# Kernel tuning notes

Measured on AMD Instinct MI355X. Metric: run time of the kernel, lower is better.

## Reference

```python
import jax, jax.numpy as jnp
import numpy as np
import math

B, N, C, H = 8, 128, 256, 8  # batch, nodes (n==m required by module), dim, heads
HD = C // H


def setup_inputs() -> dict:
    key = jax.random.key(0)
    ks = jax.random.split(key, 20)
    p = lambda k, shape: jax.random.normal(k, shape, dtype=jnp.float32) * 0.02
    inp = {
        "mol_annot": jax.random.normal(ks[0], (B, N, C), dtype=jnp.float32),
        "prot_annot": jax.random.normal(ks[1], (B, N, C), dtype=jnp.float32),
        "mol_adj": jax.random.normal(ks[2], (B, N, N, C), dtype=jnp.float32),
        "prot_adj": jax.random.normal(ks[3], (B, N, N, C), dtype=jnp.float32),
        # linear layer params (y = x @ W + b)
        "Wq": p(ks[4], (C, C)), "bq": jnp.zeros((C,), jnp.float32),
        "Wk": p(ks[5], (C, C)), "bk": jnp.zeros((C,), jnp.float32),
        "Wv": p(ks[6], (C, C)), "bv": jnp.zeros((C,), jnp.float32),
        "Wka": p(ks[7], (C, C)), "bka": jnp.zeros((C,), jnp.float32),
        "Wva": p(ks[8], (C, C)), "bva": jnp.zeros((C,), jnp.float32),
        "Wond": p(ks[9], (C, C)), "bond": jnp.zeros((C,), jnp.float32),
        "Woed": p(ks[10], (C, C)), "boed": jnp.zeros((C,), jnp.float32),
    }
    return inp


def reference(mol_annot, prot_annot, mol_adj, prot_adj,
              Wq, bq, Wk, bk, Wv, bv, Wka, bka, Wva, bva,
              Wond, bond, Woed, boed):
    b, n, c = mol_annot.shape
    h, hd = H, C // H
    inv_sqrt_dim = 1.0 / math.sqrt(c)

    q = (mol_annot @ Wq + bq).reshape(b, n, h, hd)        # [b,m,h,hd]
    k = (prot_annot @ Wk + bk).reshape(b, n, h, hd)       # [b,n,h,hd]
    v = (mol_annot @ Wv + bv).reshape(b, n, h, hd)        # [b,n,h,hd]
    mol_e = (mol_adj @ Wva + bva).reshape(b, n, n, h, hd)   # [b,m,n,h,hd]
    prot_e = (prot_adj @ Wka + bka).reshape(b, n, n, h, hd)  # [b,m,n,h,hd]

    # elementwise q*k score (full head_dim retained), gated by edge features
    attn = (q[:, :, None] * k[:, None]) * inv_sqrt_dim     # [b,m,n,h,hd]
    attn = attn * (prot_e + 1.0) * mol_e

    # edge output projection from pre-softmax scores
    mol_adj_out = attn.reshape(b, n, n, c) @ Woed + boed   # [b,m,n,c]

    # softmax over key axis (dim=2), then weighted value sum
    a = jax.nn.softmax(attn, axis=2)                       # [b,m,n,h,hd]
    node = (a * v[:, None]).sum(axis=2).reshape(b, n, c)   # [b,m,c]
    mol_annot_out = node @ Wond + bond

    return (mol_annot_out, prot_annot, mol_adj_out, prot_adj)
```

## Files before the change

kernel.cpp:

```cpp
#include <hip/hip_runtime.h>
#include <stdint.h>

constexpr int kB = 8;
constexpr int kN = 128;
constexpr int kC = 256;
#define ATTN_SCALE 0.0625f

using half8 = __attribute__((ext_vector_type(8))) _Float16;
using half4 = __attribute__((ext_vector_type(4))) _Float16;
using f32x4 = __attribute__((ext_vector_type(4))) float;

__global__ __launch_bounds__(256) void qkv_kernel(
    const float* __restrict__ mol_annot,
    const float* __restrict__ prot_annot,
    const float* __restrict__ Wq, const float* __restrict__ bq,
    const float* __restrict__ Wk, const float* __restrict__ bk,
    const float* __restrict__ Wv, const float* __restrict__ bv,
    float* __restrict__ qf, _Float16* __restrict__ kf16, float* __restrict__ vf)
{
    const int row = blockIdx.x;
    const int t   = threadIdx.x;

    __shared__ float sm[kC];
    __shared__ float sp[kC];
    sm[t] = mol_annot[row * kC + t];
    sp[t] = prot_annot[row * kC + t];
    __syncthreads();

    float aq = bq[t];
    float ak = bk[t];
    float av = bv[t];
    for (int c = 0; c < kC; ++c) {
        const float m = sm[c];
        const float p = sp[c];
        aq += m * Wq[c * kC + t];
        ak += p * Wk[c * kC + t];
        av += m * Wv[c * kC + t];
    }
    qf[row * kC + t]   = aq;
    kf16[row * kC + t] = (_Float16)ak;
    vf[row * kC + t]   = av;
}

__global__ __launch_bounds__(256) void pack_w_kernel(
    const float* __restrict__ Wva, const float* __restrict__ Wka,
    const float* __restrict__ Woed,
    _Float16* __restrict__ p_wva, _Float16* __restrict__ p_wka,
    _Float16* __restrict__ p_woed)
{
    const int blk = blockIdx.x;
    const int mat = blk >> 8;
    const int k   = blk & 255;
    const int n   = threadIdx.x;

    const float* src = (mat == 0) ? Wva : (mat == 1) ? Wka : Woed;
    _Float16*    dst = (mat == 0) ? p_wva : (mat == 1) ? p_wka : p_woed;

    const float w   = src[k * kC + n];
    const int nblk  = n >> 4;
    const int kblk  = k >> 5;
    const int lane  = (((k >> 3) & 3) << 4) | (n & 15);
    const int i     = k & 7;
    dst[(size_t)(((nblk * 8) + kblk) * 64 + lane) * 8 + i] = (_Float16)w;
}

__global__ __launch_bounds__(512, 2) void main_kernel(
    const float* __restrict__ mol_adj,
    const float* __restrict__ prot_adj,
    const float* __restrict__ bka, const float* __restrict__ bva,
    const float* __restrict__ Wond, const float* __restrict__ bond,
    const float* __restrict__ boed,
    const _Float16* __restrict__ p_wva, const _Float16* __restrict__ p_wka,
    const _Float16* __restrict__ p_woed,
    const float* __restrict__ qf, const _Float16* __restrict__ kf16,
    const float* __restrict__ vf,
    float* __restrict__ out_node,
    float* __restrict__ out_edge)
{
    const int bm   = blockIdx.x;
    const int b    = bm >> 7;
    const int tid  = threadIdx.x;
    const int lane = tid & 63;
    const int wave = tid >> 6;
    const int wm   = wave >> 2;
    const int wn   = wave & 3;
    const int lr   = lane & 15;
    const int lk   = (lane >> 4) << 3;
    const int lg4  = (lane >> 4) << 2;

    __shared__ __align__(16) _Float16 s_stage[2][kN][136];
    _Float16 (*s_attn)[264] = reinterpret_cast<_Float16 (*)[264]>(&s_stage[0][0][0]);
    __shared__ float s_red[6][kC];
    __shared__ float s_node[kC];

    float qs[4], bva_c[4], bka_c[4], boed_c[4];
    int   colv[4];
    #pragma unroll
    for (int ni = 0; ni < 4; ++ni) {
        const int c = wn * 64 + ni * 16 + lr;
        colv[ni]   = c;
        qs[ni]     = qf[(size_t)bm * kC + c] * ATTN_SCALE;
        bva_c[ni]  = bva[c];
        bka_c[ni]  = bka[c];
        boed_c[ni] = boed[c];
    }

    const float* madj = mol_adj  + (size_t)bm * kN * kC;
    const float* padj = prot_adj + (size_t)bm * kN * kC;

    f32x4 accme[4][4], accpe[4][4];
    #pragma unroll
    for (int mi = 0; mi < 4; ++mi)
        #pragma unroll
        for (int ni = 0; ni < 4; ++ni) { accme[mi][ni] = (f32x4)0.0f; accpe[mi][ni] = (f32x4)0.0f; }

    for (int kc = 0; kc < 2; ++kc) {
        #pragma unroll
        for (int v = 0; v < 8; ++v) {
            const int e   = tid + v * 512;
            const int row = e >> 5;
            const int c4  = e & 31;
            const float4 fm = *(const float4*)(madj + row * kC + kc * 128 + c4 * 4);
            const float4 fp = *(const float4*)(padj + row * kC + kc * 128 + c4 * 4);
            half4 hm, hp;
            hm[0] = (_Float16)fm.x; hm[1] = (_Float16)fm.y;
            hm[2] = (_Float16)fm.z; hm[3] = (_Float16)fm.w;
            hp[0] = (_Float16)fp.x; hp[1] = (_Float16)fp.y;
            hp[2] = (_Float16)fp.z; hp[3] = (_Float16)fp.w;
            *(half4*)&s_stage[0][row][c4 * 4] = hm;
            *(half4*)&s_stage[1][row][c4 * 4] = hp;
        }
        __syncthreads();

        #pragma unroll
        for (int kk = 0; kk < 4; ++kk) {
            const int kblk = kc * 4 + kk;
            half8 am[4], ap[4], bvf[4], bkf[4];
            #pragma unroll
            for (int mi = 0; mi < 4; ++mi) {
                const int r = wm * 64 + mi * 16 + lr;
                am[mi] = *(const half8*)&s_stage[0][r][kk * 32 + lk];
                ap[mi] = *(const half8*)&s_stage[1][r][kk * 32 + lk];
            }
            #pragma unroll
            for (int ni = 0; ni < 4; ++ni) {
                const size_t off = ((size_t)((wn * 4 + ni) * 8 + kblk) * 64 + lane) * 8;
                bvf[ni] = *(const half8*)&p_wva[off];
                bkf[ni] = *(const half8*)&p_wka[off];
            }
            #pragma unroll
            for (int mi = 0; mi < 4; ++mi)
                #pragma unroll
                for (int ni = 0; ni < 4; ++ni) {
                    accme[mi][ni] = __builtin_amdgcn_mfma_f32_16x16x32_f16(am[mi], bvf[ni], accme[mi][ni], 0, 0, 0);
                    accpe[mi][ni] = __builtin_amdgcn_mfma_f32_16x16x32_f16(ap[mi], bkf[ni], accpe[mi][ni], 0, 0, 0);
                }
        }
        __syncthreads();
    }

    const _Float16* kbase = kf16 + (size_t)b * kN * kC;
    #pragma unroll
    for (int mi = 0; mi < 4; ++mi) {
        #pragma unroll
        for (int ni = 0; ni < 4; ++ni) {
            #pragma unroll
            for (int r = 0; r < 4; ++r) {
                const int row = wm * 64 + mi * 16 + lg4 + r;
                const float kvv = (float)kbase[row * kC + colv[ni]];
                const float me  = accme[mi][ni][r] + bva_c[ni];
                const float pe  = accpe[mi][ni][r] + bka_c[ni];
                const float a   = qs[ni] * kvv * (pe + 1.0f) * me;
                s_attn[row][colv[ni]] = (_Float16)a;
            }
        }
    }
    __syncthreads();

    f32x4 acco[4][4];
    #pragma unroll
    for (int mi = 0; mi < 4; ++mi)
        #pragma unroll
        for (int ni = 0; ni < 4; ++ni) acco[mi][ni] = (f32x4)0.0f;

    #pragma unroll
    for (int kk = 0; kk < 8; ++kk) {
        half8 aa[4], bo[4];
        #pragma unroll
        for (int mi = 0; mi < 4; ++mi)
            aa[mi] = *(const half8*)&s_attn[wm * 64 + mi * 16 + lr][kk * 32 + lk];
        #pragma unroll
        for (int ni = 0; ni < 4; ++ni)
            bo[ni] = *(const half8*)&p_woed[((size_t)((wn * 4 + ni) * 8 + kk) * 64 + lane) * 8];
        #pragma unroll
        for (int mi = 0; mi < 4; ++mi)
            #pragma unroll
            for (int ni = 0; ni < 4; ++ni)
                acco[mi][ni] = __builtin_amdgcn_mfma_f32_16x16x32_f16(aa[mi], bo[ni], acco[mi][ni], 0, 0, 0);
    }

    float* oe = out_edge + (size_t)bm * kN * kC;
    #pragma unroll
    for (int mi = 0; mi < 4; ++mi)
        #pragma unroll
        for (int ni = 0; ni < 4; ++ni)
            #pragma unroll
            for (int r = 0; r < 4; ++r) {
                const int row = wm * 64 + mi * 16 + lg4 + r;
                oe[(size_t)row * kC + colv[ni]] = acco[mi][ni][r] + boed_c[ni];
            }

    {
        const int c  = tid & 255;
        const int hh = tid >> 8;
        const int r0 = hh * 64;

        float mx = -1.0e30f;
        #pragma unroll 4
        for (int r = 0; r < 64; ++r) mx = fmaxf(mx, (float)s_attn[r0 + r][c]);
        s_red[hh][c] = mx;
        __syncthreads();
        mx = fmaxf(s_red[0][c], s_red[1][c]);

        const float* vbase = vf + (size_t)b * kN * kC;
        float ssum = 0.0f, sacc = 0.0f;
        #pragma unroll 4
        for (int r = 0; r < 64; ++r) {
            const float a = (float)s_attn[r0 + r][c];
            const float e = __expf(a - mx);
            ssum += e;
            sacc += e * vbase[(size_t)(r0 + r) * kC + c];
        }
        s_red[2 + hh][c] = ssum;
        s_red[4 + hh][c] = sacc;
        __syncthreads();
        if (tid < 256) {
            s_node[tid] = (s_red[4][tid] + s_red[5][tid]) /
                          (s_red[2][tid] + s_red[3][tid]);
        }
        __syncthreads();
    }

    if (tid < 256) {
        float acc = bond[tid];
        const float4* sn4 = reinterpret_cast<const float4*>(s_node);
        for (int c4 = 0; c4 < 64; ++c4) {
            const float4 nv = sn4[c4];
            acc += nv.x * Wond[(c4 * 4 + 0) * kC + tid];
            acc += nv.y * Wond[(c4 * 4 + 1) * kC + tid];
            acc += nv.z * Wond[(c4 * 4 + 2) * kC + tid];
            acc += nv.w * Wond[(c4 * 4 + 3) * kC + tid];
        }
        out_node[(size_t)bm * kC + tid] = acc;
    }
}

extern "C" void kernel_launch(void* const* d_in, const int* in_sizes, int n_in,
                              void* d_out, int out_size, void* d_ws, size_t ws_size,
                              hipStream_t stream)
{
    const float* mol_annot  = (const float*)d_in[0];
    const float* prot_annot = (const float*)d_in[1];
    const float* mol_adj    = (const float*)d_in[2];
    const float* prot_adj   = (const float*)d_in[3];
    const float* Wq  = (const float*)d_in[4];
    const float* bq  = (const float*)d_in[5];
    const float* Wk  = (const float*)d_in[6];
    const float* bk  = (const float*)d_in[7];
    const float* Wv  = (const float*)d_in[8];
    const float* bv  = (const float*)d_in[9];
    const float* Wka = (const float*)d_in[10];
    const float* bka = (const float*)d_in[11];
    const float* Wva = (const float*)d_in[12];
    const float* bva = (const float*)d_in[13];
    const float* Wond = (const float*)d_in[14];
    const float* bond = (const float*)d_in[15];
    const float* Woed = (const float*)d_in[16];
    const float* boed = (const float*)d_in[17];

    float*    qf    = (float*)d_ws;
    float*    vf    = qf + (size_t)kB * kN * kC;
    _Float16* kf16  = (_Float16*)(vf + (size_t)kB * kN * kC);
    _Float16* p_wva = kf16 + (size_t)kB * kN * kC;
    _Float16* p_wka = p_wva + (size_t)kC * kC;
    _Float16* p_woed = p_wka + (size_t)kC * kC;

    float* out  = (float*)d_out;
    float* out0 = out;
    float* out1 = out + (size_t)kB * kN * kC;
    float* out2 = out + (size_t)2 * kB * kN * kC;
    float* out3 = out2 + (size_t)kB * kN * kN * kC;

    hipMemcpyAsync(out1, prot_annot, (size_t)kB * kN * kC * sizeof(float),
                   hipMemcpyDeviceToDevice, stream);
    hipMemcpyAsync(out3, prot_adj, (size_t)kB * kN * kN * kC * sizeof(float),
                   hipMemcpyDeviceToDevice, stream);

    qkv_kernel<<<dim3(kB * kN), dim3(256), 0, stream>>>(
        mol_annot, prot_annot, Wq, bq, Wk, bk, Wv, bv, qf, kf16, vf);

    pack_w_kernel<<<dim3(3 * kC), dim3(256), 0, stream>>>(
        Wva, Wka, Woed, p_wva, p_wka, p_woed);

    main_kernel<<<dim3(kB * kN), dim3(512), 0, stream>>>(
        mol_adj, prot_adj, bka, bva, Wond, bond, boed,
        p_wva, p_wka, p_woed, qf, kf16, vf, out0, out2);
}
```

Baseline: 678.7 us.

## Fuse passthrough copies into kernels and serialize edge GEMMs to raise occupancy

Drops the two device-to-device memcpys and writes the prot_annot and prot_adj passthrough outputs from inside qkv_kernel and main_kernel while those tensors are already being read. This saves a separate full read of the large prot_adj tensor. The main kernel now runs the prot_e and mol_e projections one after the other with a single accumulator set and a small 32-wide staging buffer. This cuts registers and LDS so launch bounds can go from 2 to 4 blocks. Edge output is staged through LDS for coalesced float4 stores, and the k-loop now has more barriers per block.

```diff
diff --git a/kernel.cpp b/kernel.cpp
--- a/kernel.cpp
+++ b/kernel.cpp
@@ -16,15 +16,18 @@
     const float* __restrict__ Wq, const float* __restrict__ bq,
     const float* __restrict__ Wk, const float* __restrict__ bk,
     const float* __restrict__ Wv, const float* __restrict__ bv,
-    float* __restrict__ qf, _Float16* __restrict__ kf16, float* __restrict__ vf)
+    float* __restrict__ qf, _Float16* __restrict__ kf16, float* __restrict__ vf,
+    float* __restrict__ out1)
 {
     const int row = blockIdx.x;
     const int t   = threadIdx.x;
 
     __shared__ float sm[kC];
     __shared__ float sp[kC];
+    const float pv = prot_annot[row * kC + t];
     sm[t] = mol_annot[row * kC + t];
-    sp[t] = prot_annot[row * kC + t];
+    sp[t] = pv;
+    out1[row * kC + t] = pv;
     __syncthreads();
 
     float aq = bq[t];
@@ -64,7 +67,7 @@
     dst[(size_t)(((nblk * 8) + kblk) * 64 + lane) * 8 + i] = (_Float16)w;
 }
 
-__global__ __launch_bounds__(512, 2) void main_kernel(
+__global__ __launch_bounds__(512, 4) void main_kernel(
     const float* __restrict__ mol_adj,
     const float* __restrict__ prot_adj,
     const float* __restrict__ bka, const float* __restrict__ bva,
@@ -75,7 +78,8 @@
     const float* __restrict__ qf, const _Float16* __restrict__ kf16,
     const float* __restrict__ vf,
     float* __restrict__ out_node,
-    float* __restrict__ out_edge)
+    float* __restrict__ out_edge,
+    float* __restrict__ out3)
 {
     const int bm   = blockIdx.x;
     const int b    = bm >> 7;
@@ -88,127 +92,135 @@
     const int lk   = (lane >> 4) << 3;
     const int lg4  = (lane >> 4) << 2;
 
-    __shared__ __align__(16) _Float16 s_stage[2][kN][136];
-    _Float16 (*s_attn)[264] = reinterpret_cast<_Float16 (*)[264]>(&s_stage[0][0][0]);
-    __shared__ float s_red[6][kC];
-    __shared__ float s_node[kC];
-
-    float qs[4], bva_c[4], bka_c[4], boed_c[4];
-    int   colv[4];
-    #pragma unroll
-    for (int ni = 0; ni < 4; ++ni) {
-        const int c = wn * 64 + ni * 16 + lr;
-        colv[ni]   = c;
-        qs[ni]     = qf[(size_t)bm * kC + c] * ATTN_SCALE;
-        bva_c[ni]  = bva[c];
-        bka_c[ni]  = bka[c];
-        boed_c[ni] = boed[c];
-    }
+    __shared__ __align__(16) _Float16 s_attn[kN][264];
+    __shared__ __align__(16) _Float16 s_stage[kN][40];
+    float (*s_red)[kC] = reinterpret_cast<float (*)[kC]>(&s_stage[0][0]);
+    float (*s_oe)[260] = reinterpret_cast<float (*)[260]>(&s_attn[0][0]);
 
     const float* madj = mol_adj  + (size_t)bm * kN * kC;
     const float* padj = prot_adj + (size_t)bm * kN * kC;
-
-    f32x4 accme[4][4], accpe[4][4];
+    float*       o3   = out3     + (size_t)bm * kN * kC;
+
+    const int srow = tid >> 3;
+    const int sc4  = (tid & 7) * 4;
+
+    f32x4 acc[4][4];
+
     #pragma unroll
     for (int mi = 0; mi < 4; ++mi)
         #pragma unroll
-        for (int ni = 0; ni < 4; ++ni) { accme[mi][ni] = (f32x4)0.0f; accpe[mi][ni] = (f32x4)0.0f; }
-
-    for (int kc = 0; kc < 2; ++kc) {
-        #pragma unroll
-        for (int v = 0; v < 8; ++v) {
-            const int e   = tid + v * 512;
-            const int row = e >> 5;
-            const int c4  = e & 31;
-            const float4 fm = *(const float4*)(madj + row * kC + kc * 128 + c4 * 4);
-            const float4 fp = *(const float4*)(padj + row * kC + kc * 128 + c4 * 4);
-            half4 hm, hp;
-            hm[0] = (_Float16)fm.x; hm[1] = (_Float16)fm.y;
-            hm[2] = (_Float16)fm.z; hm[3] = (_Float16)fm.w;
-            hp[0] = (_Float16)fp.x; hp[1] = (_Float16)fp.y;
-            hp[2] = (_Float16)fp.z; hp[3] = (_Float16)fp.w;
-            *(half4*)&s_stage[0][row][c4 * 4] = hm;
-            *(half4*)&s_stage[1][row][c4 * 4] = hp;
-        }
-        __syncthreads();
-
-        #pragma unroll
-        for (int kk = 0; kk < 4; ++kk) {
-            const int kblk = kc * 4 + kk;
-            half8 am[4], ap[4], bvf[4], bkf[4];
-            #pragma unroll
-            for (int mi = 0; mi < 4; ++mi) {
-                const int r = wm * 64 + mi * 16 + lr;
-                am[mi] = *(const half8*)&s_stage[0][r][kk * 32 + lk];
-                ap[mi] = *(const half8*)&s_stage[1][r][kk * 32 + lk];
-            }
-            #pragma unroll
-            for (int ni = 0; ni < 4; ++ni) {
-                const size_t off = ((size_t)((wn * 4 + ni) * 8 + kblk) * 64 + lane) * 8;
-                bvf[ni] = *(const half8*)&p_wva[off];
-                bkf[ni] = *(const half8*)&p_wka[off];
-            }
+        for (int ni = 0; ni < 4; ++ni) acc[mi][ni] = (f32x4)0.0f;
+
+    for (int kc = 0; kc < 8; ++kc) {
+        #pragma unroll
+        for (int v = 0; v < 2; ++v) {
+            const int r = srow + v * 64;
+            const float4 f = *(const float4*)(padj + r * kC + kc * 32 + sc4);
+            *(float4*)(o3 + r * kC + kc * 32 + sc4) = f;
+            half4 h;
+            h[0] = (_Float16)f.x; h[1] = (_Float16)f.y;
+            h[2] = (_Float16)f.z; h[3] = (_Float16)f.w;
+            *(half4*)&s_stage[r][sc4] = h;
+        }
+        __syncthreads();
+
+        half8 af[4];
+        #pragma unroll
+        for (int mi = 0; mi < 4; ++mi)
+            af[mi] = *(const half8*)&s_stage[wm * 64 + mi * 16 + lr][lk];
+        #pragma unroll
+        for (int ni = 0; ni < 4; ++ni) {
+            const half8 bf = *(const half8*)&p_wka[((size_t)((wn * 4 + ni) * 8 + kc) * 64 + lane) * 8];
+            #pragma unroll
+            for (int mi = 0; mi < 4; ++mi)
+                acc[mi][ni] = __builtin_amdgcn_mfma_f32_16x16x32_f16(af[mi], bf, acc[mi][ni], 0, 0, 0);
+        }
+        __syncthreads();
+    }
+
+    #pragma unroll
+    for (int ni = 0; ni < 4; ++ni) {
+        const int col = wn * 64 + ni * 16 + lr;
+        const float bk_c = bka[col] + 1.0f;
+        #pragma unroll
+        for (int mi = 0; mi < 4; ++mi)
+            #pragma unroll
+            for (int r = 0; r < 4; ++r)
+                s_attn[wm * 64 + mi * 16 + lg4 + r][col] = (_Float16)(acc[mi][ni][r] + bk_c);
+    }
+
+    #pragma unroll
+    for (int mi = 0; mi < 4; ++mi)
+        #pragma unroll
+        for (int ni = 0; ni < 4; ++ni) acc[mi][ni] = (f32x4)0.0f;
+
+    for (int kc = 0; kc < 8; ++kc) {
+        #pragma unroll
+        for (int v = 0; v < 2; ++v) {
+            const int r = srow + v * 64;
+            const float4 f = *(const float4*)(madj + r * kC + kc * 32 + sc4);
+            half4 h;
+            h[0] = (_Float16)f.x; h[1] = (_Float16)f.y;
+            h[2] = (_Float16)f.z; h[3] = (_Float16)f.w;
+            *(half4*)&s_stage[r][sc4] = h;
+        }
+        __syncthreads();
+
+        half8 af[4];
+        #pragma unroll
+        for (int mi = 0; mi < 4; ++mi)
+            af[mi] = *(const half8*)&s_stage[wm * 64 + mi * 16 + lr][lk];
+        #pragma unroll
+        for (int ni = 0; ni < 4; ++ni) {
+            const half8 bf = *(const half8*)&p_wva[((size_t)((wn * 4 + ni) * 8 + kc) * 64 + lane) * 8];
+            #pragma unroll
+            for (int mi = 0; mi < 4; ++mi)
+                acc[mi][ni] = __builtin_amdgcn_mfma_f32_16x16x32_f16(af[mi], bf, acc[mi][ni], 0, 0, 0);
+        }
+        __syncthreads();
+    }
+
+    {
+        const _Float16* kb  = kf16 + (size_t)b * kN * kC;
+        const float*   qrow = qf   + (size_t)bm * kC;
+        #pragma unroll
+        for (int ni = 0; ni < 4; ++ni) {
+            const int col = wn * 64 + ni * 16 + lr;
+            const float qs   = qrow[col] * ATTN_SCALE;
+            const float bv_c = bva[col];
             #pragma unroll
             for (int mi = 0; mi < 4; ++mi)
                 #pragma unroll
-                for (int ni = 0; ni < 4; ++ni) {
-                    accme[mi][ni] = __builtin_amdgcn_mfma_f32_16x16x32_f16(am[mi], bvf[ni], accme[mi][ni], 0, 0, 0);
-                    accpe[mi][ni] = __builtin_amdgcn_mfma_f32_16x16x32_f16(ap[mi], bkf[ni], accpe[mi][ni], 0, 0, 0);
+                for (int r = 0; r < 4; ++r) {
+                    const int row = wm * 64 + mi * 16 + lg4 + r;
+                    const float kvv = (float)kb[row * kC + col];
+                    const float ppe = (float)s_attn[row][col];
+                    const float me  = acc[mi][ni][r] + bv_c;
+                    s_attn[row][col] = (_Float16)(qs * kvv * ppe * me);
                 }
         }
-        __syncthreads();
-    }
-
-    const _Float16* kbase = kf16 + (size_t)b * kN * kC;
-    #pragma unroll
-    for (int mi = 0; mi < 4; ++mi) {
-        #pragma unroll
-        for (int ni = 0; ni < 4; ++ni) {
-            #pragma unroll
-            for (int r = 0; r < 4; ++r) {
-                const int row = wm * 64 + mi * 16 + lg4 + r;
-                const float kvv = (float)kbase[row * kC + colv[ni]];
-                const float me  = accme[mi][ni][r] + bva_c[ni];
-                const float pe  = accpe[mi][ni][r] + bka_c[ni];
-                const float a   = qs[ni] * kvv * (pe + 1.0f) * me;
-                s_attn[row][colv[ni]] = (_Float16)a;
-            }
-        }
     }
     __syncthreads();
 
-    f32x4 acco[4][4];
     #pragma unroll
     for (int mi = 0; mi < 4; ++mi)
         #pragma unroll
-        for (int ni = 0; ni < 4; ++ni) acco[mi][ni] = (f32x4)0.0f;
+        for (int ni = 0; ni < 4; ++ni) acc[mi][ni] = (f32x4)0.0f;
 
     #pragma unroll
     for (int kk = 0; kk < 8; ++kk) {
-        half8 aa[4], bo[4];
+        half8 aa[4];
         #pragma unroll
         for (int mi = 0; mi < 4; ++mi)
             aa[mi] = *(const half8*)&s_attn[wm * 64 + mi * 16 + lr][kk * 32 + lk];
         #pragma unroll
-        for (int ni = 0; ni < 4; ++ni)
-            bo[ni] = *(const half8*)&p_woed[((size_t)((wn * 4 + ni) * 8 + kk) * 64 + lane) * 8];
-        #pragma unroll
-        for (int mi = 0; mi < 4; ++mi)
-            #pragma unroll
-            for (int ni = 0; ni < 4; ++ni)
-                acco[mi][ni] = __builtin_amdgcn_mfma_f32_16x16x32_f16(aa[mi], bo[ni], acco[mi][ni], 0, 0, 0);
-    }
-
-    float* oe = out_edge + (size_t)bm * kN * kC;
-    #pragma unroll
-    for (int mi = 0; mi < 4; ++mi)
-        #pragma unroll
-        for (int ni = 0; ni < 4; ++ni)
-            #pragma unroll
-            for (int r = 0; r < 4; ++r) {
-                const int row = wm * 64 + mi * 16 + lg4 + r;
-                oe[(size_t)row * kC + colv[ni]] = acco[mi][ni][r] + boed_c[ni];
-            }
+        for (int ni = 0; ni < 4; ++ni) {
+            const half8 bo = *(const half8*)&p_woed[((size_t)((wn * 4 + ni) * 8 + kk) * 64 + lane) * 8];
+            #pragma unroll
+            for (int mi = 0; mi < 4; ++mi)
+                acc[mi][ni] = __builtin_amdgcn_mfma_f32_16x16x32_f16(aa[mi], bo, acc[mi][ni], 0, 0, 0);
+        }
+    }
 
     {
         const int c  = tid & 255;
@@ -222,36 +234,65 @@
         __syncthreads();
         mx = fmaxf(s_red[0][c], s_red[1][c]);
 
-        const float* vbase = vf + (size_t)b * kN * kC;
+        const float* vb = vf + (size_t)b * kN * kC;
         float ssum = 0.0f, sacc = 0.0f;
         #pragma unroll 4
         for (int r = 0; r < 64; ++r) {
             const float a = (float)s_attn[r0 + r][c];
             const float e = __expf(a - mx);
             ssum += e;
-            sacc += e * vbase[(size_t)(r0 + r) * kC + c];
+            sacc += e * vb[(size_t)(r0 + r) * kC + c];
         }
         s_red[2 + hh][c] = ssum;
         s_red[4 + hh][c] = sacc;
         __syncthreads();
         if (tid < 256) {
-            s_node[tid] = (s_red[4][tid] + s_red[5][tid]) /
-                          (s_red[2][tid] + s_red[3][tid]);
-        }
-        __syncthreads();
+            s_red[6][tid] = (s_red[4][tid] + s_red[5][tid]) /
+                            (s_red[2][tid] + s_red[3][tid]);
+        }
+    }
+    __syncthreads();
+
+    {
+        float* oe = out_edge + (size_t)bm * kN * kC;
+        #pragma unroll
+        for (int h = 0; h < 2; ++h) {
+            if (wm == h) {
+                #pragma unroll
+                for (int ni = 0; ni < 4; ++ni) {
+                    const int col = wn * 64 + ni * 16 + lr;
+                    const float bo_c = boed[col];
+                    #pragma unroll
+                    for (int mi = 0; mi < 4; ++mi)
+                        #pragma unroll
+                        for (int r = 0; r < 4; ++r)
+                            s_oe[mi * 16 + lg4 + r][col] = acc[mi][ni][r] + bo_c;
+                }
+            }
+            __syncthreads();
+            #pragma unroll
+            for (int v = 0; v < 8; ++v) {
+                const int e   = v * 512 + tid;
+                const int row = e >> 6;
+                const int c4  = (e & 63) * 4;
+                const float4 val = *(const float4*)&s_oe[row][c4];
+                *(float4*)(oe + (size_t)(h * 64 + row) * kC + c4) = val;
+            }
+            __syncthreads();
+        }
     }
 
     if (tid < 256) {
-        float acc = bond[tid];
-        const float4* sn4 = reinterpret_cast<const float4*>(s_node);
+        float accn = bond[tid];
+        const float4* sn4 = reinterpret_cast<const float4*>(&s_red[6][0]);
         for (int c4 = 0; c4 < 64; ++c4) {
             const float4 nv = sn4[c4];
-            acc += nv.x * Wond[(c4 * 4 + 0) * kC + tid];
-            acc += nv.y * Wond[(c4 * 4 + 1) * kC + tid];
-            acc += nv.z * Wond[(c4 * 4 + 2) * kC + tid];
-            acc += nv.w * Wond[(c4 * 4 + 3) * kC + tid];
-        }
-        out_node[(size_t)bm * kC + tid] = acc;
+            accn += nv.x * Wond[(c4 * 4 + 0) * kC + tid];
+            accn += nv.y * Wond[(c4 * 4 + 1) * kC + tid];
+            accn += nv.z * Wond[(c4 * 4 + 2) * kC + tid];
+            accn += nv.w * Wond[(c4 * 4 + 3) * kC + tid];
+        }
+        out_node[(size_t)bm * kC + tid] = accn;
     }
 }
 
@@ -278,11 +319,11 @@
     const float* Woed = (const float*)d_in[16];
     const float* boed = (const float*)d_in[17];
 
-    float*    qf    = (float*)d_ws;
-    float*    vf    = qf + (size_t)kB * kN * kC;
-    _Float16* kf16  = (_Float16*)(vf + (size_t)kB * kN * kC);
-    _Float16* p_wva = kf16 + (size_t)kB * kN * kC;
-    _Float16* p_wka = p_wva + (size_t)kC * kC;
+    float*    qf     = (float*)d_ws;
+    float*    vf     = qf + (size_t)kB * kN * kC;
+    _Float16* kf16   = (_Float16*)(vf + (size_t)kB * kN * kC);
+    _Float16* p_wva  = kf16 + (size_t)kB * kN * kC;
+    _Float16* p_wka  = p_wva + (size_t)kC * kC;
     _Float16* p_woed = p_wka + (size_t)kC * kC;
 
     float* out  = (float*)d_out;
@@ -291,18 +332,13 @@
     float* out2 = out + (size_t)2 * kB * kN * kC;
     float* out3 = out2 + (size_t)kB * kN * kN * kC;
 
-    hipMemcpyAsync(out1, prot_annot, (size_t)kB * kN * kC * sizeof(float),
-                   hipMemcpyDeviceToDevice, stream);
-    hipMemcpyAsync(out3, prot_adj, (size_t)kB * kN * kN * kC * sizeof(float),
-                   hipMemcpyDeviceToDevice, stream);
-
     qkv_kernel<<<dim3(kB * kN), dim3(256), 0, stream>>>(
-        mol_annot, prot_annot, Wq, bq, Wk, bk, Wv, bv, qf, kf16, vf);
+        mol_annot, prot_annot, Wq, bq, Wk, bk, Wv, bv, qf, kf16, vf, out1);
 
     pack_w_kernel<<<dim3(3 * kC), dim3(256), 0, stream>>>(
         Wva, Wka, Woed, p_wva, p_wka, p_woed);
 
     main_kernel<<<dim3(kB * kN), dim3(512), 0, stream>>>(
         mol_adj, prot_adj, bka, bva, Wond, bond, boed,
-        p_wva, p_wka, p_woed, qf, kf16, vf, out0, out2);
+        p_wva, p_wka, p_woed, qf, kf16, vf, out0, out2, out3);
 }
```

Measured after the change: 611.2 us. -9.9%, faster.
